# Optimization experiments

Hardware: AMD Instinct MI355X
Metric: run time of the kernel (lower is better)

Reference implementation:

```python
import jax, jax.numpy as jnp
import numpy as np

N, E, IN_FEATS, HID, HEADS = 50000, 800000, 256, 32, 8
NEG_SLOPE = 0.2


def _init_params(key):
    ks = jax.random.split(key, 12)
    def lin(k, fi, fo):
        return jax.random.normal(k, (fi, fo), jnp.float32) * (1.0 / np.sqrt(fi))
    p = {}
    # layer 0: in_feats -> HID x HEADS
    p['W0'] = lin(ks[0], IN_FEATS, HEADS * HID)
    p['al0'] = jax.random.normal(ks[1], (HEADS, HID), jnp.float32) * 0.1
    p['ar0'] = jax.random.normal(ks[2], (HEADS, HID), jnp.float32) * 0.1
    p['b0'] = jnp.zeros((HEADS * HID,), jnp.float32)
    # layer 1: HID*HEADS -> HID x HEADS
    p['W1'] = lin(ks[3], HEADS * HID, HEADS * HID)
    p['al1'] = jax.random.normal(ks[4], (HEADS, HID), jnp.float32) * 0.1
    p['ar1'] = jax.random.normal(ks[5], (HEADS, HID), jnp.float32) * 0.1
    p['b1'] = jnp.zeros((HEADS * HID,), jnp.float32)
    # layer 2 (final): HID*HEADS -> HID x 1 head, no activation
    p['W2'] = lin(ks[6], HEADS * HID, HID)
    p['al2'] = jax.random.normal(ks[7], (1, HID), jnp.float32) * 0.1
    p['ar2'] = jax.random.normal(ks[8], (1, HID), jnp.float32) * 0.1
    p['b2'] = jnp.zeros((HID,), jnp.float32)
    return p


def setup_inputs() -> dict:
    key = jax.random.key(0)
    k1, k2, k3, kp = jax.random.split(key, 4)
    inp = {
        'features': jax.random.normal(k1, (N, IN_FEATS), jnp.float32),
        'src': jax.random.randint(k2, (E,), 0, N, jnp.int32),
        'dst': jax.random.randint(k3, (E,), 0, N, jnp.int32),
    }
    inp.update(_init_params(kp))
    return inp


def _gat_layer(x, src, dst, W, al, ar, b, heads, act):
    n = x.shape[0]
    d = W.shape[1] // heads
    feat = (x @ W).reshape(n, heads, d)           # [N,H,D]
    el = jnp.sum(feat * al, axis=-1)              # [N,H]
    er = jnp.sum(feat * ar, axis=-1)              # [N,H]
    e = jax.nn.leaky_relu(el[src] + er[dst], NEG_SLOPE)   # [E,H]
    # segment softmax over destination neighborhoods
    emax = jax.ops.segment_max(e, dst, num_segments=n)
    ex = jnp.exp(e - emax[dst])
    denom = jax.ops.segment_sum(ex, dst, num_segments=n)
    a = ex / (denom[dst] + 1e-9)                  # [E,H]
    msg = feat[src] * a[:, :, None]               # [E,H,D]
    out = jax.ops.segment_sum(msg, dst, num_segments=n)   # [N,H,D]
    out = out + b.reshape(1, heads, d)
    return act(out) if act is not None else out


def reference(features, src, dst, W0, al0, ar0, b0, W1, al1, ar1, b1, W2, al2, ar2, b2):
    h = _gat_layer(features, src, dst, W0, al0, ar0, b0, HEADS, jax.nn.elu)
    h = h.reshape(h.shape[0], -1)
    h = _gat_layer(h, src, dst, W1, al1, ar1, b1, HEADS, jax.nn.elu)
    h = h.reshape(h.shape[0], -1)
    h = _gat_layer(h, src, dst, W2, al2, ar2, b2, 1, None)   # [N,1,D]
    return h.mean(axis=1)                                    # [N,D]
```

## Files before the change

kernel.cpp:

```cpp
#include <hip/hip_runtime.h>

typedef unsigned short u16;
typedef unsigned int   u32;
typedef __attribute__((ext_vector_type(8))) short  short8;
typedef __attribute__((ext_vector_type(4))) float  f32x4;
typedef __attribute__((ext_vector_type(2))) float  f32x2;
typedef __attribute__((ext_vector_type(2))) unsigned int u32v2;
typedef __attribute__((ext_vector_type(4))) unsigned int u32v4;

#define NN 50000
#define NE 800000

__device__ __forceinline__ float bf2f(u16 b) { return __uint_as_float(((u32)b) << 16); }
__device__ __forceinline__ float bflo(u32 p) { return __uint_as_float(p << 16); }
__device__ __forceinline__ float bfhi(u32 p) { return __uint_as_float(p & 0xffff0000u); }
__device__ __forceinline__ u16 f2bf(float f) {
    u32 u = __float_as_uint(f);
    u32 r = u + 0x7fffu + ((u >> 16) & 1u);
    return (u16)(r >> 16);
}
__device__ __forceinline__ float lexp(float v) {
    v = fmaxf(v, 0.2f * v);
    return __expf(fminf(v, 60.f));
}

__device__ __forceinline__ int block_detect(const u32* x, int n, int* sh, int* sz) {
    int t = threadIdx.x;
    int hits = 0, nz = 0;
    for (int i = t; i < n; i += 256) {
        u32 w = x[i];
        if (w) {
            ++nz;
            u32 e = (w >> 7) & 0xffu;
            if (e >= 100 && e <= 150) ++hits;
        }
    }
    sh[t] = hits; sz[t] = nz;
    __syncthreads();
    for (int ofs = 128; ofs > 0; ofs >>= 1) {
        if (t < ofs) { sh[t] += sh[t + ofs]; sz[t] += sz[t + ofs]; }
        __syncthreads();
    }
    return (sz[0] == 0) ? 2 : ((sh[0] * 2 >= sz[0]) ? 0 : 1);
}

struct PrepArgs {
    const u32* dp[13]; int dnw[13];
    const void* cs[9]; float* cd[9]; int cn[9];
    const void* wsrc[3]; u16* wdst[3]; int wN[3]; int wchunks[3];
};

__global__ __launch_bounds__(256) void k_prep(PrepArgs a, int* flags) {
    __shared__ int sh[256], sz[256];
    const int bid = blockIdx.x;
    const int t = threadIdx.x;
    if (bid < 13) {
        int f = block_detect(a.dp[bid], a.dnw[bid], sh, sz);
        if (t == 0) flags[bid] = f;
    } else if (bid < 22) {
        const int j = bid - 13;
        int nw = a.cn[j] / 2; if (nw > 512) nw = 512;
        const int fl = block_detect((const u32*)a.cs[j], nw, sh, sz);
        if (t < a.cn[j]) {
            float v = 0.f;
            if (fl == 1) v = ((const float*)a.cs[j])[t];
            else if (fl == 0) v = bf2f(((const u16*)a.cs[j])[t]);
            a.cd[j][t] = v;
        }
    } else {
        int wj, base;
        if (bid < 54)      { wj = 0; base = 22; }
        else if (bid < 86) { wj = 1; base = 54; }
        else               { wj = 2; base = 86; }
        const void* Wsrc = a.wsrc[wj];
        const int fl = block_detect((const u32*)Wsrc, 512, sh, sz);
        const int id = (bid - base) * 256 + t;
        if (id < a.wchunks[wj]) {
            const int L = id & 63, kt = (id >> 6) & 7, nt = id >> 9;
            const int col = nt * 16 + (L & 15);
            const int krow = kt * 32 + ((L >> 4) & 3) * 8;
            const bool isf32 = (fl == 1);
            const int N = a.wN[wj];
            u16* Wp = a.wdst[wj];
#pragma unroll
            for (int j2 = 0; j2 < 8; ++j2) {
                int s = (krow + j2) * N + col;
                Wp[id * 8 + j2] = isf32 ? f2bf(((const float*)Wsrc)[s])
                                        : ((const u16*)Wsrc)[s];
            }
        }
    }
}

__global__ void k_hist(const int* __restrict__ dst, int* __restrict__ deg, int E) {
    int e = blockIdx.x * 256 + threadIdx.x;
    if (e < E) atomicAdd(&deg[dst[e]], 1);
}

__global__ __launch_bounds__(256) void k_scan_partial(const int* __restrict__ deg,
                                                      int* __restrict__ bsum, int n) {
    __shared__ int red[256];
    int t = threadIdx.x;
    int i = blockIdx.x * 256 + t;
    red[t] = (i < n) ? deg[i] : 0;
    __syncthreads();
    for (int ofs = 128; ofs > 0; ofs >>= 1) {
        if (t < ofs) red[t] += red[t + ofs];
        __syncthreads();
    }
    if (t == 0) bsum[blockIdx.x] = red[0];
}

__global__ __launch_bounds__(256) void k_scan_bsum(int* __restrict__ bsum, int nb) {
    __shared__ int s[256];
    int t = threadIdx.x;
    int v = (t < nb) ? bsum[t] : 0;
    s[t] = v;
    __syncthreads();
    for (int ofs = 1; ofs < 256; ofs <<= 1) {
        int x = (t >= ofs) ? s[t - ofs] : 0;
        __syncthreads();
        s[t] += x;
        __syncthreads();
    }
    if (t < nb) bsum[t] = s[t] - v;
}

__global__ __launch_bounds__(256) void k_scan_final(const int* __restrict__ deg,
                                                    const int* __restrict__ bsum,
                                                    int* __restrict__ rowptr,
                                                    int* __restrict__ cursor, int n) {
    __shared__ int s[256];
    int t = threadIdx.x;
    int i = blockIdx.x * 256 + t;
    int v = (i < n) ? deg[i] : 0;
    s[t] = v;
    __syncthreads();
    for (int ofs = 1; ofs < 256; ofs <<= 1) {
        int x = (t >= ofs) ? s[t - ofs] : 0;
        __syncthreads();
        s[t] += x;
        __syncthreads();
    }
    int excl = bsum[blockIdx.x] + s[t] - v;
    if (i < n) {
        rowptr[i] = excl;
        cursor[i] = excl;
        if (i == n - 1) rowptr[n] = excl + v;
    }
}

__global__ void k_scatter(const int* __restrict__ src, const int* __restrict__ dst,
                          int* __restrict__ cursor, int* __restrict__ csr_src, int E) {
    int e = blockIdx.x * 256 + threadIdx.x;
    if (e >= E) return;
    int p = atomicAdd(&cursor[dst[e]], 1);
    csr_src[p] = src[e];
}

__global__ __launch_bounds__(512) void k_gemm_mfma(const void* __restrict__ Xv,
                                                   const int* __restrict__ xflag,
                                                   const u16* __restrict__ Wp,
                                                   u16* __restrict__ OUT, int nrows) {
    __shared__ u16 As[64 * 256];
    const int t = threadIdx.x;
    const int w = t >> 6, L = t & 63;
    const int quad = (L >> 4) & 3;
    const int r0 = blockIdx.x * 64;
    const bool xf32 = (xflag != nullptr) && (*xflag == 1);

    short8* Asv = (short8*)As;
    short8 zero = {0, 0, 0, 0, 0, 0, 0, 0};
#pragma unroll
    for (int i = 0; i < 4; ++i) {
        int g = i * 512 + t;
        int row = g >> 5, cc = g & 31;
        int r = r0 + row;
        short8 val = zero;
        if (r < nrows) {
            if (xf32) {
                const f32x4* Xf4 = (const f32x4*)Xv;
                f32x4 lo = Xf4[(size_t)r * 64 + cc * 2];
                f32x4 hi = Xf4[(size_t)r * 64 + cc * 2 + 1];
                val[0] = (short)f2bf(lo[0]); val[1] = (short)f2bf(lo[1]);
                val[2] = (short)f2bf(lo[2]); val[3] = (short)f2bf(lo[3]);
                val[4] = (short)f2bf(hi[0]); val[5] = (short)f2bf(hi[1]);
                val[6] = (short)f2bf(hi[2]); val[7] = (short)f2bf(hi[3]);
            } else {
                val = ((const short8*)Xv)[(size_t)r * 32 + cc];
            }
        }
        Asv[cc * 64 + (row ^ (cc & 7))] = val;
    }

    const short8* Wv = (const short8*)Wp;
    short8 bf[2][8];
#pragma unroll
    for (int jn = 0; jn < 2; ++jn) {
        int nt = w + jn * 8;
#pragma unroll
        for (int kt = 0; kt < 8; ++kt) bf[jn][kt] = Wv[(nt * 8 + kt) * 64 + L];
    }
    __syncthreads();

    f32x4 acc[4][2];
#pragma unroll
    for (int mi = 0; mi < 4; ++mi)
#pragma unroll
        for (int jn = 0; jn < 2; ++jn) acc[mi][jn] = (f32x4){0.f, 0.f, 0.f, 0.f};

#pragma unroll
    for (int kt = 0; kt < 8; ++kt) {
        const int ccr = kt * 4 + quad;
#pragma unroll
        for (int mi = 0; mi < 4; ++mi) {
            short8 af = Asv[ccr * 64 + ((mi * 16 + (L & 15)) ^ (ccr & 7))];
            acc[mi][0] = __builtin_amdgcn_mfma_f32_16x16x32_bf16(af, bf[0][kt], acc[mi][0], 0, 0, 0);
            acc[mi][1] = __builtin_amdgcn_mfma_f32_16x16x32_bf16(af, bf[1][kt], acc[mi][1], 0, 0, 0);
        }
    }

#pragma unroll
    for (int mi = 0; mi < 4; ++mi) {
        int rb = r0 + mi * 16 + quad * 4;
#pragma unroll
        for (int jn = 0; jn < 2; ++jn) {
            int c = (w + jn * 8) * 16 + (L & 15);
#pragma unroll
            for (int reg = 0; reg < 4; ++reg) {
                int r = rb + reg;
                if (r < nrows) OUT[(size_t)r * 256 + c] = f2bf(acc[mi][jn][reg]);
            }
        }
    }
}

__global__ __launch_bounds__(256) void k_gemm_mfma32(const u16* __restrict__ Xb,
                                                     const u16* __restrict__ Wp,
                                                     u16* __restrict__ OUT, int nrows) {
    __shared__ u16 As[128 * 256];
    const int t = threadIdx.x;
    const int w = t >> 6, L = t & 63;
    const int quad = (L >> 4) & 3;
    const int r0 = blockIdx.x * 128;
    const int mh = (w >> 1) * 64, nt = w & 1;

    const short8* Xv = (const short8*)Xb;
    short8* Asv = (short8*)As;
    short8 zero = {0, 0, 0, 0, 0, 0, 0, 0};
#pragma unroll
    for (int i = 0; i < 16; ++i) {
        int g = i * 256 + t;
        int row = g >> 5, cc = g & 31;
        int r = r0 + row;
        Asv[cc * 128 + (row ^ (cc & 7))] = (r < nrows) ? Xv[(size_t)r * 32 + cc] : zero;
    }

    const short8* Wv = (const short8*)Wp;
    short8 bf[8];
#pragma unroll
    for (int kt = 0; kt < 8; ++kt) bf[kt] = Wv[(nt * 8 + kt) * 64 + L];
    __syncthreads();

    f32x4 acc[4];
#pragma unroll
    for (int mi = 0; mi < 4; ++mi) acc[mi] = (f32x4){0.f, 0.f, 0.f, 0.f};

#pragma unroll
    for (int kt = 0; kt < 8; ++kt) {
        const int ccr = kt * 4 + quad;
#pragma unroll
        for (int mi = 0; mi < 4; ++mi) {
            short8 af = Asv[ccr * 128 + ((mh + mi * 16 + (L & 15)) ^ (ccr & 7))];
            acc[mi] = __builtin_amdgcn_mfma_f32_16x16x32_bf16(af, bf[kt], acc[mi], 0, 0, 0);
        }
    }

#pragma unroll
    for (int mi = 0; mi < 4; ++mi) {
        int rb = r0 + mh + mi * 16 + quad * 4;
        int c = nt * 16 + (L & 15);
#pragma unroll
        for (int reg = 0; reg < 4; ++reg) {
            int r = rb + reg;
            if (r < nrows) OUT[(size_t)r * 32 + c] = f2bf(acc[mi][reg]);
        }
    }
}

__global__ void k_elr8(const u16* __restrict__ featb, const float* __restrict__ al,
                       const float* __restrict__ ar, float* __restrict__ el,
                       float* __restrict__ er, int n) {
    int idx = blockIdx.x * 256 + threadIdx.x;
    if (idx >= n * 8) return;
    int node = idx >> 3, h = idx & 7;
    const u32v4* fu = (const u32v4*)((const u32*)featb + (size_t)node * 128 + h * 16);
    const float* A = al + h * 32;
    const float* B = ar + h * 32;
    float sl = 0.f, sr = 0.f;
#pragma unroll
    for (int j = 0; j < 4; ++j) {
        u32v4 w4 = fu[j];
#pragma unroll
        for (int k = 0; k < 4; ++k) {
            u32 w = (k == 0) ? w4.x : (k == 1) ? w4.y : (k == 2) ? w4.z : w4.w;
            float f0 = bflo(w), f1 = bfhi(w);
            int c = j * 8 + k * 2;
            sl += f0 * A[c] + f1 * A[c + 1];
            sr += f0 * B[c] + f1 * B[c + 1];
        }
    }
    el[idx] = sl;
    er[idx] = sr;
}

__global__ void k_elr1(const u16* __restrict__ featb, const float* __restrict__ al,
                       const float* __restrict__ ar, float* __restrict__ el,
                       float* __restrict__ er, int n) {
    int node = blockIdx.x * 256 + threadIdx.x;
    if (node >= n) return;
    const u32v4* fu = (const u32v4*)((const u32*)featb + (size_t)node * 16);
    float sl = 0.f, sr = 0.f;
#pragma unroll
    for (int j = 0; j < 4; ++j) {
        u32v4 w4 = fu[j];
#pragma unroll
        for (int k = 0; k < 4; ++k) {
            u32 w = (k == 0) ? w4.x : (k == 1) ? w4.y : (k == 2) ? w4.z : w4.w;
            float f0 = bflo(w), f1 = bfhi(w);
            int c = j * 8 + k * 2;
            sl += f0 * al[c] + f1 * al[c + 1];
            sr += f0 * ar[c] + f1 * ar[c + 1];
        }
    }
    el[node] = sl;
    er[node] = sr;
}

__global__ __launch_bounds__(256) void k_gather8(const int* __restrict__ rowptr,
                                                 const int* __restrict__ csr_src,
                                                 const float* __restrict__ el,
                                                 const float* __restrict__ er,
                                                 const u32v2* __restrict__ featb4,
                                                 const float* __restrict__ bias,
                                                 u32v2* __restrict__ xout4) {
    __shared__ __align__(16) float sAL[4][2][64];
    __shared__ __align__(16) int   sSL[4][2][8];
    const int t = threadIdx.x;
    const int wv = t >> 6;
    const int q = t & 63;
    const int d = blockIdx.x * 4 + wv;
    const int eL = q >> 3, hL = q & 7;
    const int b = rowptr[d], e = rowptr[d + 1];
    const int deg = e - b;
    const int nch = (deg + 7) >> 3;
    const float erA = er[d * 8 + hL];

    float (*AL)[64] = sAL[wv];
    int (*SL)[8] = sSL[wv];

    float a0 = 0.f, a1 = 0.f, a2 = 0.f, a3 = 0.f;
    float partial = 0.f;

    u32v2 fw[8], fw2[8];
    int csrP = 0, ncP = 0;
    float elP = 0.f;

    if (nch > 0) {
        const int nc0 = deg < 8 ? deg : 8;
        const int i0 = eL < nc0 ? eL : nc0 - 1;
        const int s0 = csr_src[b + i0];
        if (nch > 1) {
            const int r1 = deg - 8;
            ncP = r1 < 8 ? r1 : 8;
            const int i1 = eL < ncP ? eL : ncP - 1;
            csrP = csr_src[b + 8 + i1];
        }
        const float el0 = el[s0 * 8 + hL];
        if (hL == 0) SL[0][eL] = s0;
        const int4 sv0 = *(const int4*)&SL[0][0];
        const int4 sv1 = *(const int4*)&SL[0][4];
        fw[0] = featb4[sv0.x * 64 + q];
        fw[1] = featb4[sv0.y * 64 + q];
        fw[2] = featb4[sv0.z * 64 + q];
        fw[3] = featb4[sv0.w * 64 + q];
        fw[4] = featb4[sv1.x * 64 + q];
        fw[5] = featb4[sv1.y * 64 + q];
        fw[6] = featb4[sv1.z * 64 + q];
        fw[7] = featb4[sv1.w * 64 + q];
        const float ex0 = (eL < nc0) ? lexp(el0 + erA) : 0.f;
        partial += ex0;
        AL[0][hL * 8 + eL] = ex0;
        if (nch > 1) elP = el[csrP * 8 + hL];
    }

    for (int c = 0; c < nch; ++c) {
        const int cur = c & 1, nxt = cur ^ 1;

        int csrF = 0, ncF = 0;
        if (c + 2 < nch) {
            const int r2 = deg - (c + 2) * 8;
            ncF = r2 < 8 ? r2 : 8;
            const int i2 = eL < ncF ? eL : ncF - 1;
            csrF = csr_src[b + (c + 2) * 8 + i2];
        }

        if (c + 1 < nch) {
            if (hL == 0) SL[nxt][eL] = csrP;
            const int4 sv0 = *(const int4*)&SL[nxt][0];
            const int4 sv1 = *(const int4*)&SL[nxt][4];
            fw2[0] = featb4[sv0.x * 64 + q];
            fw2[1] = featb4[sv0.y * 64 + q];
            fw2[2] = featb4[sv0.z * 64 + q];
            fw2[3] = featb4[sv0.w * 64 + q];
            fw2[4] = featb4[sv1.x * 64 + q];
            fw2[5] = featb4[sv1.y * 64 + q];
            fw2[6] = featb4[sv1.z * 64 + q];
            fw2[7] = featb4[sv1.w * 64 + q];
            const float exN = (eL < ncP) ? lexp(elP + erA) : 0.f;
            partial += exN;
            AL[nxt][hL * 8 + eL] = exN;
        }

        const int h8 = (q >> 3) * 8;
        const f32x4 A0 = *(const f32x4*)&AL[cur][h8];
        const f32x4 A1 = *(const f32x4*)&AL[cur][h8 + 4];

        if (c + 2 < nch) elP = el[csrF * 8 + hL];

#define GAT_EDGE(i, axv) { const u32v2 w_ = fw[i]; \
        a0 += bflo(w_.x) * (axv); a1 += bfhi(w_.x) * (axv); \
        a2 += bflo(w_.y) * (axv); a3 += bfhi(w_.y) * (axv); }
        GAT_EDGE(0, A0[0]) GAT_EDGE(1, A0[1]) GAT_EDGE(2, A0[2]) GAT_EDGE(3, A0[3])
        GAT_EDGE(4, A1[0]) GAT_EDGE(5, A1[1]) GAT_EDGE(6, A1[2]) GAT_EDGE(7, A1[3])
#undef GAT_EDGE

#pragma unroll
        for (int i = 0; i < 8; ++i) fw[i] = fw2[i];
        csrP = csrF;
        ncP = ncF;
    }

    float v = partial;
    v += __shfl_xor(v, 8);
    v += __shfl_xor(v, 16);
    v += __shfl_xor(v, 32);
    const float ssd = __shfl(v, q >> 3);

    const float rd = 1.f / (ssd + 1e-9f);
    const float4 bb = *(const float4*)&bias[4 * q];
    float v0 = a0 * rd + bb.x;
    float v1 = a1 * rd + bb.y;
    float v2 = a2 * rd + bb.z;
    float v3 = a3 * rd + bb.w;
    v0 = v0 > 0.f ? v0 : expm1f(v0);
    v1 = v1 > 0.f ? v1 : expm1f(v1);
    v2 = v2 > 0.f ? v2 : expm1f(v2);
    v3 = v3 > 0.f ? v3 : expm1f(v3);
    u32v2 o;
    o.x = (u32)f2bf(v0) | ((u32)f2bf(v1) << 16);
    o.y = (u32)f2bf(v2) | ((u32)f2bf(v3) << 16);
    xout4[(size_t)d * 64 + q] = o;
}

__global__ __launch_bounds__(256) void k_gather1(const int* __restrict__ rowptr,
                                                 const int* __restrict__ csr_src,
                                                 const float* __restrict__ el,
                                                 const float* __restrict__ er,
                                                 const u32* __restrict__ featb2,
                                                 const float* __restrict__ bias,
                                                 void* __restrict__ out,
                                                 const int* __restrict__ flag, int n) {
    int t = threadIdx.x;
    int d = blockIdx.x * 16 + (t >> 4);
    int q = t & 15;
    if (d >= n) return;
    int b = rowptr[d], e = rowptr[d + 1];
    float erd = er[d];
    float a0 = 0.f, a1 = 0.f, ssum = 0.f;
    int p = b;
    for (; p + 4 <= e; p += 4) {
        int s0 = csr_src[p], s1 = csr_src[p + 1], s2 = csr_src[p + 2], s3 = csr_src[p + 3];
        float e0 = lexp(el[s0] + erd);
        float e1 = lexp(el[s1] + erd);
        float e2 = lexp(el[s2] + erd);
        float e3 = lexp(el[s3] + erd);
        u32 w0 = featb2[(size_t)s0 * 16 + q];
        u32 w1 = featb2[(size_t)s1 * 16 + q];
        u32 w2 = featb2[(size_t)s2 * 16 + q];
        u32 w3 = featb2[(size_t)s3 * 16 + q];
        a0 += bflo(w0) * e0; a1 += bfhi(w0) * e0;
        a0 += bflo(w1) * e1; a1 += bfhi(w1) * e1;
        a0 += bflo(w2) * e2; a1 += bfhi(w2) * e2;
        a0 += bflo(w3) * e3; a1 += bfhi(w3) * e3;
        ssum += (e0 + e1) + (e2 + e3);
    }
    for (; p < e; ++p) {
        int s = csr_src[p];
        float ev = lexp(el[s] + erd);
        u32 w = featb2[(size_t)s * 16 + q];
        a0 += bflo(w) * ev;
        a1 += bfhi(w) * ev;
        ssum += ev;
    }
    float rd = 1.f / (ssum + 1e-9f);
    float v0 = a0 * rd + bias[2 * q];
    float v1 = a1 * rd + bias[2 * q + 1];
    if (*flag == 1) {
        f32x2 o = {v0, v1};
        ((f32x2*)out)[(size_t)d * 16 + q] = o;
    } else {
        ((u32*)out)[(size_t)d * 16 + q] = (u32)f2bf(v0) | ((u32)f2bf(v1) << 16);
    }
}

extern "C" void kernel_launch(void* const* d_in, const int* in_sizes, int n_in,
                              void* d_out, int out_size, void* d_ws, size_t ws_size,
                              hipStream_t stream) {
    const void* features = d_in[0];
    const int* src = (const int*)d_in[1];
    const int* dst = (const int*)d_in[2];

    char* ws = (char*)d_ws;
    size_t off = 0;
    auto carve = [&](size_t bytes) -> void* {
        void* p = ws + off;
        off = (off + bytes + 255) & ~(size_t)255;
        return p;
    };
    int*   flags = (int*)carve(64);
    float* pconv = (float*)carve(2048 * 4);
    u16*   Wp0 = (u16*)carve(65536 * 2);
    u16*   Wp1 = (u16*)carve(65536 * 2);
    u16*   Wp2 = (u16*)carve(8192 * 2);
    u16*   Xb    = (u16*)carve((size_t)NN * 256 * 2);
    u16*   featb = (u16*)carve((size_t)NN * 256 * 2);
    float* el   = (float*)carve((size_t)NN * 8 * 4);
    float* er   = (float*)carve((size_t)NN * 8 * 4);
    int*   deg     = (int*)carve((size_t)NN * 4);
    int*   cursor  = (int*)carve((size_t)NN * 4);
    int*   rowptr  = (int*)carve((size_t)(NN + 1) * 4);
    int*   bsum    = (int*)carve(256 * 4);
    int*   csr_src = (int*)carve((size_t)NE * 4);
    if (off > ws_size) return;

    const int N = NN, E = NE;
    const int nscan = (N + 255) / 256;

    PrepArgs pa;
    const int din_idx[13] = {0, 3, 4, 5, 6, 7, 8, 9, 10, 11, 12, 13, 14};
    for (int j = 0; j < 13; ++j) {
        pa.dp[j] = (const u32*)d_in[din_idx[j]];
        int nw = in_sizes[din_idx[j]] / 2;
        pa.dnw[j] = nw > 512 ? 512 : nw;
    }
    const int psl[9] = {4, 5, 6, 8, 9, 10, 12, 13, 14};
    float* dsts[9];
    {
        size_t o = 0;
        for (int j = 0; j < 9; ++j) {
            dsts[j] = pconv + o;
            o += (size_t)in_sizes[psl[j]];
        }
    }
    for (int j = 0; j < 9; ++j) {
        pa.cs[j] = d_in[psl[j]];
        pa.cd[j] = dsts[j];
        pa.cn[j] = in_sizes[psl[j]];
    }
    pa.wsrc[0] = d_in[3];  pa.wdst[0] = Wp0; pa.wN[0] = 256; pa.wchunks[0] = 8192;
    pa.wsrc[1] = d_in[7];  pa.wdst[1] = Wp1; pa.wN[1] = 256; pa.wchunks[1] = 8192;
    pa.wsrc[2] = d_in[11]; pa.wdst[2] = Wp2; pa.wN[2] = 32;  pa.wchunks[2] = 1024;
    k_prep<<<90, 256, 0, stream>>>(pa, flags);
    float* al0f = dsts[0]; float* ar0f = dsts[1]; float* b0f = dsts[2];
    float* al1f = dsts[3]; float* ar1f = dsts[4]; float* b1f = dsts[5];
    float* al2f = dsts[6]; float* ar2f = dsts[7]; float* b2f = dsts[8];

    hipMemsetAsync(deg, 0, (size_t)N * 4, stream);
    k_hist<<<(E + 255) / 256, 256, 0, stream>>>(dst, deg, E);
    k_scan_partial<<<nscan, 256, 0, stream>>>(deg, bsum, N);
    k_scan_bsum<<<1, 256, 0, stream>>>(bsum, nscan);
    k_scan_final<<<nscan, 256, 0, stream>>>(deg, bsum, rowptr, cursor, N);
    k_scatter<<<(E + 255) / 256, 256, 0, stream>>>(src, dst, cursor, csr_src, E);

    const int ggrid = (N + 63) / 64;

    k_gemm_mfma<<<ggrid, 512, 0, stream>>>(features, flags, Wp0, featb, N);
    k_elr8<<<(N * 8 + 255) / 256, 256, 0, stream>>>(featb, al0f, ar0f, el, er, N);
    k_gather8<<<N / 4, 256, 0, stream>>>(rowptr, csr_src, el, er,
                                         (const u32v2*)featb, b0f, (u32v2*)Xb);

    k_gemm_mfma<<<ggrid, 512, 0, stream>>>(Xb, nullptr, Wp1, featb, N);
    k_elr8<<<(N * 8 + 255) / 256, 256, 0, stream>>>(featb, al1f, ar1f, el, er, N);
    k_gather8<<<N / 4, 256, 0, stream>>>(rowptr, csr_src, el, er,
                                         (const u32v2*)featb, b1f, (u32v2*)Xb);

    k_gemm_mfma32<<<(N + 127) / 128, 256, 0, stream>>>(Xb, Wp2, featb, N);
    k_elr1<<<(N + 255) / 256, 256, 0, stream>>>(featb, al2f, ar2f, el, er, N);
    k_gather1<<<(N + 15) / 16, 256, 0, stream>>>(rowptr, csr_src, el, er,
                                                 (const u32*)featb, b2f,
                                                 d_out, flags, N);
}
```

Before: 418.4 us.

## Cooperatively load edges in final-layer gather and fold degree memset into prep

Measured after the change: 421.5 us. No clear change (+0.8%).

```diff
diff --git a/kernel.cpp b/kernel.cpp
--- a/kernel.cpp
+++ b/kernel.cpp
@@ -48,6 +48,7 @@
     const u32* dp[13]; int dnw[13];
     const void* cs[9]; float* cd[9]; int cn[9];
     const void* wsrc[3]; u16* wdst[3]; int wN[3]; int wchunks[3];
+    int* deg; int degn;
 };
 
 __global__ __launch_bounds__(256) void k_prep(PrepArgs a, int* flags) {
@@ -67,7 +68,7 @@
             else if (fl == 0) v = bf2f(((const u16*)a.cs[j])[t]);
             a.cd[j][t] = v;
         }
-    } else {
+    } else if (bid < 90) {
         int wj, base;
         if (bid < 54)      { wj = 0; base = 22; }
         else if (bid < 86) { wj = 1; base = 54; }
@@ -89,6 +90,9 @@
                                         : ((const u16*)Wsrc)[s];
             }
         }
+    } else {
+        const int i = (bid - 90) * 256 + t;
+        if (i < a.degn) a.deg[i] = 0;
     }
 }
 
@@ -471,46 +475,42 @@
                                                  const float* __restrict__ bias,
                                                  void* __restrict__ out,
                                                  const int* __restrict__ flag, int n) {
-    int t = threadIdx.x;
-    int d = blockIdx.x * 16 + (t >> 4);
-    int q = t & 15;
+    const int t = threadIdx.x;
+    const int d = blockIdx.x * 16 + (t >> 4);
+    const int lane = t & 15;
     if (d >= n) return;
-    int b = rowptr[d], e = rowptr[d + 1];
-    float erd = er[d];
+    const int b = rowptr[d], e = rowptr[d + 1];
+    const float erd = er[d];
     float a0 = 0.f, a1 = 0.f, ssum = 0.f;
-    int p = b;
-    for (; p + 4 <= e; p += 4) {
-        int s0 = csr_src[p], s1 = csr_src[p + 1], s2 = csr_src[p + 2], s3 = csr_src[p + 3];
-        float e0 = lexp(el[s0] + erd);
-        float e1 = lexp(el[s1] + erd);
-        float e2 = lexp(el[s2] + erd);
-        float e3 = lexp(el[s3] + erd);
-        u32 w0 = featb2[(size_t)s0 * 16 + q];
-        u32 w1 = featb2[(size_t)s1 * 16 + q];
-        u32 w2 = featb2[(size_t)s2 * 16 + q];
-        u32 w3 = featb2[(size_t)s3 * 16 + q];
-        a0 += bflo(w0) * e0; a1 += bfhi(w0) * e0;
-        a0 += bflo(w1) * e1; a1 += bfhi(w1) * e1;
-        a0 += bflo(w2) * e2; a1 += bfhi(w2) * e2;
-        a0 += bflo(w3) * e3; a1 += bfhi(w3) * e3;
-        ssum += (e0 + e1) + (e2 + e3);
-    }
-    for (; p < e; ++p) {
-        int s = csr_src[p];
-        float ev = lexp(el[s] + erd);
-        u32 w = featb2[(size_t)s * 16 + q];
-        a0 += bflo(w) * ev;
-        a1 += bfhi(w) * ev;
-        ssum += ev;
-    }
-    float rd = 1.f / (ssum + 1e-9f);
-    float v0 = a0 * rd + bias[2 * q];
-    float v1 = a1 * rd + bias[2 * q + 1];
+
+    for (int c = b; c < e; c += 16) {
+        const int idx = c + lane;
+        const int s_own = csr_src[idx < e ? idx : e - 1];
+        const float ex_own = (idx < e) ? lexp(el[s_own] + erd) : 0.f;
+        ssum += ex_own;
+#pragma unroll
+        for (int i = 0; i < 16; ++i) {
+            const int si = __shfl(s_own, i, 16);
+            const float ai = __shfl(ex_own, i, 16);
+            const u32 w = featb2[(size_t)si * 16 + lane];
+            a0 += bflo(w) * ai;
+            a1 += bfhi(w) * ai;
+        }
+    }
+
+    ssum += __shfl_xor(ssum, 1);
+    ssum += __shfl_xor(ssum, 2);
+    ssum += __shfl_xor(ssum, 4);
+    ssum += __shfl_xor(ssum, 8);
+
+    const float rd = 1.f / (ssum + 1e-9f);
+    const float v0 = a0 * rd + bias[2 * lane];
+    const float v1 = a1 * rd + bias[2 * lane + 1];
     if (*flag == 1) {
         f32x2 o = {v0, v1};
-        ((f32x2*)out)[(size_t)d * 16 + q] = o;
+        ((f32x2*)out)[(size_t)d * 16 + lane] = o;
     } else {
-        ((u32*)out)[(size_t)d * 16 + q] = (u32)f2bf(v0) | ((u32)f2bf(v1) << 16);
+        ((u32*)out)[(size_t)d * 16 + lane] = (u32)f2bf(v0) | ((u32)f2bf(v1) << 16);
     }
 }
 
@@ -571,12 +571,12 @@
     pa.wsrc[0] = d_in[3];  pa.wdst[0] = Wp0; pa.wN[0] = 256; pa.wchunks[0] = 8192;
     pa.wsrc[1] = d_in[7];  pa.wdst[1] = Wp1; pa.wN[1] = 256; pa.wchunks[1] = 8192;
     pa.wsrc[2] = d_in[11]; pa.wdst[2] = Wp2; pa.wN[2] = 32;  pa.wchunks[2] = 1024;
-    k_prep<<<90, 256, 0, stream>>>(pa, flags);
+    pa.deg = deg; pa.degn = N;
+    k_prep<<<90 + nscan, 256, 0, stream>>>(pa, flags);
     float* al0f = dsts[0]; float* ar0f = dsts[1]; float* b0f = dsts[2];
     float* al1f = dsts[3]; float* ar1f = dsts[4]; float* b1f = dsts[5];
     float* al2f = dsts[6]; float* ar2f = dsts[7]; float* b2f = dsts[8];
 
-    hipMemsetAsync(deg, 0, (size_t)N * 4, stream);
     k_hist<<<(E + 255) / 256, 256, 0, stream>>>(dst, deg, E);
     k_scan_partial<<<nscan, 256, 0, stream>>>(deg, bsum, N);
     k_scan_bsum<<<1, 256, 0, stream>>>(bsum, nscan);
```
